# Optimization experiments

Measured on AMD Instinct MI355X. Metric: run time of the kernel, lower is better.

Reference implementation:

```python
import jax, jax.numpy as jnp
import numpy as np

N_PATCHES = 14
PS = 16            # patch size: 224 / 14
C, H_IMG, W_IMG = 3, 224, 224
HIDDEN = 768
HEADS = 12
DH = HIDDEN // HEADS
BLOCKS = 12
MLP = 4 * HIDDEN
OUT = 1000
SEQ = N_PATCHES ** 2 + 1  # 197
BATCH = 64


def get_positional_embeddings(seq_len, d):
    # sin(i/10000^(j/d)) for even j, cos(i/10000^((j-1)/d)) for odd j
    i = jnp.arange(seq_len, dtype=jnp.float32)[:, None]
    j = jnp.arange(d)[None, :]
    even = (j % 2 == 0)
    expo = jnp.where(even, j, j - 1).astype(jnp.float32) / d
    ang = i / (10000.0 ** expo)
    return jnp.where(even, jnp.sin(ang), jnp.cos(ang))


def layernorm(x, g, b, eps=1e-5):
    mu = x.mean(-1, keepdims=True)
    var = ((x - mu) ** 2).mean(-1, keepdims=True)
    return (x - mu) / jnp.sqrt(var + eps) * g + b


def mhsa(x, qw, qb, kw, kb, vw, vb):
    # x: [B,S,HIDDEN]; per-head linears qw/kw/vw: [H,DH,DH] (torch Linear weight layout)
    B, S, _ = x.shape
    xh = x.reshape(B, S, HEADS, DH)
    q = jnp.einsum('bshd,hed->bshe', xh, qw) + qb
    k = jnp.einsum('bshd,hed->bshe', xh, kw) + kb
    v = jnp.einsum('bshd,hed->bshe', xh, vw) + vb
    scores = jnp.einsum('bshe,bthe->bhst', q, k) / jnp.sqrt(jnp.float32(DH))
    attn = jax.nn.softmax(scores, axis=-1)
    out = jnp.einsum('bhst,bthe->bshe', attn, v)
    return out.reshape(B, S, HIDDEN)


def vit_block(x, p):
    ln1_g, ln1_b, qw, qb, kw, kb, vw, vb, ln2_g, ln2_b, w1, b1, w2, b2 = p
    x = x + mhsa(layernorm(x, ln1_g, ln1_b), qw, qb, kw, kb, vw, vb)
    h = layernorm(x, ln2_g, ln2_b)
    h = jax.nn.gelu(h @ w1.T + b1, approximate=False) @ w2.T + b2
    return x + h


def patchify(images):
    # [N,C,H,W] -> [N, n_patches^2, C*PS*PS], channel-major within each patch
    n = images.shape[0]
    x = images.reshape(n, C, N_PATCHES, PS, N_PATCHES, PS)
    x = x.transpose(0, 2, 4, 1, 3, 5)  # n, pi, pj, c, ps, ps
    return x.reshape(n, N_PATCHES * N_PATCHES, C * PS * PS)


def setup_inputs() -> dict:
    key = jax.random.key(0)
    ks = jax.random.split(key, 20)
    s = 0.02
    return {
        'images': jax.random.normal(ks[0], (BATCH, C, H_IMG, W_IMG), jnp.float32),
        'mapper_w': jax.random.normal(ks[1], (HIDDEN, C * PS * PS), jnp.float32) * s,
        'mapper_b': jnp.zeros((HIDDEN,), jnp.float32),
        'cls_token': jax.random.uniform(ks[2], (1, HIDDEN), jnp.float32),
        'ln1_g': jnp.ones((BLOCKS, HIDDEN), jnp.float32),
        'ln1_b': jnp.zeros((BLOCKS, HIDDEN), jnp.float32),
        'qw': jax.random.normal(ks[3], (BLOCKS, HEADS, DH, DH), jnp.float32) * s,
        'qb': jnp.zeros((BLOCKS, HEADS, DH), jnp.float32),
        'kw': jax.random.normal(ks[4], (BLOCKS, HEADS, DH, DH), jnp.float32) * s,
        'kb': jnp.zeros((BLOCKS, HEADS, DH), jnp.float32),
        'vw': jax.random.normal(ks[5], (BLOCKS, HEADS, DH, DH), jnp.float32) * s,
        'vb': jnp.zeros((BLOCKS, HEADS, DH), jnp.float32),
        'ln2_g': jnp.ones((BLOCKS, HIDDEN), jnp.float32),
        'ln2_b': jnp.zeros((BLOCKS, HIDDEN), jnp.float32),
        'w1': jax.random.normal(ks[6], (BLOCKS, MLP, HIDDEN), jnp.float32) * s,
        'b1': jnp.zeros((BLOCKS, MLP), jnp.float32),
        'w2': jax.random.normal(ks[7], (BLOCKS, HIDDEN, MLP), jnp.float32) * s,
        'b2': jnp.zeros((BLOCKS, HIDDEN), jnp.float32),
        'head_w': jax.random.normal(ks[8], (OUT, HIDDEN), jnp.float32) * s,
        'head_b': jnp.zeros((OUT,), jnp.float32),
    }


def reference(images, mapper_w, mapper_b, cls_token, ln1_g, ln1_b, qw, qb, kw, kb,
              vw, vb, ln2_g, ln2_b, w1, b1, w2, b2, head_w, head_b):
    n = images.shape[0]
    patches = patchify(images)
    tokens = patches @ mapper_w.T + mapper_b                      # [B, 196, HIDDEN]
    cls = jnp.broadcast_to(cls_token[None], (n, 1, HIDDEN))
    tokens = jnp.concatenate([cls, tokens], axis=1)               # [B, 197, HIDDEN]
    out = tokens + get_positional_embeddings(SEQ, HIDDEN)[None]

    stacked = (ln1_g, ln1_b, qw, qb, kw, kb, vw, vb, ln2_g, ln2_b, w1, b1, w2, b2)

    def step(x, p):
        return vit_block(x, p), None

    out, _ = jax.lax.scan(step, out, stacked)
    cls_out = out[:, 0]                                           # [B, HIDDEN]
    return jax.nn.softmax(cls_out @ head_w.T + head_b, axis=-1)
```

## Files before the change

kernel.cpp:

```cpp
#include <hip/hip_runtime.h>
#include <cstdint>
#include <cstddef>
#include <cstdio>

using u16 = unsigned short;
using u32 = unsigned int;

typedef __attribute__((ext_vector_type(8))) __bf16 bf16x8;
typedef __attribute__((ext_vector_type(4))) float f32x4;

struct alignas(16) U128 { u32 w[4]; };
struct alignas(16) F4   { float x[4]; };
struct alignas(8)  US4  { u16 h[4]; };

#define DEVFN static __device__ __forceinline__

DEVFN u16 f2bf(float x) {
  union { float f; u32 u; } v; v.f = x;
  u32 r = v.u + 0x7fffu + ((v.u >> 16) & 1u);
  return (u16)(r >> 16);
}

DEVFN bf16x8 ld16(const u16* p) { return __builtin_bit_cast(bf16x8, *(const U128*)p); }

DEVFN f32x4 mfma16(bf16x8 a, bf16x8 b, f32x4 c) {
  return __builtin_amdgcn_mfma_f32_16x16x32_bf16(a, b, c, 0, 0, 0);
}

DEVFN void gload_lds16(const u16* g, u16* l) {
  __builtin_amdgcn_global_load_lds(
      (const __attribute__((address_space(1))) void*)g,
      (__attribute__((address_space(3))) void*)l, 16, 0, 0);
}

DEVFN float gelu(float x) {
  float z = fabsf(x) * 0.70710678118f;
  float t = __builtin_amdgcn_rcpf(1.f + 0.3275911f * z);
  float p = t * (0.254829592f + t * (-0.284496736f + t * (1.421413741f +
            t * (-1.453152027f + t * 1.061405429f))));
  float e = __expf(-z * z);
  float erfz = 1.f - p * e;
  erfz = copysignf(erfz, x);
  return 0.5f * x * (1.f + erfz);
}

constexpr int SEQL   = 197;
constexpr int NB     = 64;
constexpr int NH     = 12;
constexpr int MROWS  = NB * SEQL;
constexpr int MPAD   = 12672;
constexpr int MPAD2  = 12800;
constexpr int MPATCH = NB * 196;
constexpr int SP     = 208;
constexpr int SP2    = 224;
constexpr int BHN    = NB * NH;

constexpr size_t OFF_X    = 0;
constexpr size_t OFF_ALN  = OFF_X    + (size_t)MPAD * 768 * 4;
constexpr size_t OFF_H    = OFF_ALN  + (size_t)MPAD2 * 768 * 2;
constexpr size_t OFF_WQKV = OFF_H    + (size_t)MPAD2 * 3072 * 2;
constexpr size_t OFF_W1   = OFF_WQKV + (size_t)2304 * 768 * 2;
constexpr size_t OFF_W2   = OFF_W1   + (size_t)3072 * 768 * 2;
constexpr size_t OFF_WMAP = OFF_W2   + (size_t)3072 * 768 * 2;
constexpr size_t OFF_Q    = OFF_WMAP + (size_t)768 * 768 * 2;
constexpr size_t OFF_K    = OFF_Q    + (size_t)BHN * SP * 64 * 2;
constexpr size_t OFF_VT   = OFF_K    + (size_t)BHN * SP * 64 * 2;
constexpr size_t OFF_PAT  = OFF_VT   + (size_t)BHN * 64 * SP2 * 2;
constexpr size_t OFF_POS  = OFF_PAT  + (size_t)MPATCH * 768 * 2;
constexpr size_t WS_NEED  = OFF_POS  + (size_t)SEQL * 768 * 4;

__global__ void zero_kernel(u32* __restrict__ p, long n) {
  long i = (long)blockIdx.x * 256 + threadIdx.x;
  long stride = (long)gridDim.x * 256;
  for (; i < n; i += stride) p[i] = 0u;
}

__global__ void cvt_kernel(const float* __restrict__ src, u16* __restrict__ dst, int n) {
  int i = blockIdx.x * 256 + threadIdx.x;
  if (i < n) dst[i] = f2bf(src[i]);
}

__global__ void pos_kernel(float* __restrict__ pos) {
  int i = blockIdx.x * 256 + threadIdx.x;
  if (i >= SEQL * 768) return;
  int s = i / 768, j = i - s * 768;
  float expo = (float)(j & ~1) * (1.0f / 768.0f);
  float ang  = (float)s * expf(-expo * logf(10000.0f));
  pos[i] = (j & 1) ? cosf(ang) : sinf(ang);
}

__global__ void cls_kernel(const float* __restrict__ cls, const float* __restrict__ pos,
                           float* __restrict__ X) {
  int b = blockIdx.x;
  for (int c = threadIdx.x; c < 768; c += 256)
    X[(size_t)b * SEQL * 768 + c] = cls[c] + pos[c];
}

__global__ void patchify_kernel(const float* __restrict__ img, u16* __restrict__ out) {
  int i = blockIdx.x * 256 + threadIdx.x;
  if (i >= MPATCH * 768) return;
  int m = i / 768, k = i - m * 768;
  int b = m / 196, p = m - b * 196;
  int py = p / 14, px = p - py * 14;
  int c = k >> 8, rem = k & 255, iy = rem >> 4, ix = rem & 15;
  float v = img[(((size_t)b * 3 + c) * 224 + py * 16 + iy) * 224 + px * 16 + ix];
  out[i] = f2bf(v);
}

__global__ void build_wqkv2(const float* __restrict__ qw, const float* __restrict__ kw,
                            const float* __restrict__ vw, u16* __restrict__ W, int blk) {
  int i = blockIdx.x * 256 + threadIdx.x;
  if (i >= 2304 * 128) return;
  int n = i >> 7, kk = i & 127;
  int p = n / 768, ef = n - p * 768;
  int h = ef >> 6, e = ef & 63;
  float v = 0.f;
  if ((kk >> 6) == (h & 1)) {
    int d = kk & 63;
    const float* w = (p == 0) ? qw : (p == 1) ? kw : vw;
    v = w[(((size_t)blk * NH + h) * 64 + e) * 64 + d];
  }
  W[i] = f2bf(v);
}

__global__ __launch_bounds__(256) void ln_kernel(const float* __restrict__ X,
    const float* __restrict__ g, const float* __restrict__ b, u16* __restrict__ out) {
  int row  = blockIdx.x * 4 + (threadIdx.x >> 6);
  int lane = threadIdx.x & 63;
  const float* x = X + (size_t)row * 768 + lane * 12;
  F4 a0 = *(const F4*)(x);
  F4 a1 = *(const F4*)(x + 4);
  F4 a2 = *(const F4*)(x + 8);
  float v[12];
  #pragma unroll
  for (int j = 0; j < 4; ++j) { v[j] = a0.x[j]; v[4 + j] = a1.x[j]; v[8 + j] = a2.x[j]; }
  float s = 0.f, q = 0.f;
  #pragma unroll
  for (int j = 0; j < 12; ++j) { s += v[j]; q += v[j] * v[j]; }
  #pragma unroll
  for (int d = 1; d < 64; d <<= 1) { s += __shfl_xor(s, d); q += __shfl_xor(q, d); }
  float mu  = s * (1.f / 768.f);
  float var = q * (1.f / 768.f) - mu * mu;
  float rs  = rsqrtf(var + 1e-5f);
  const float* gp = g + lane * 12;
  const float* bp = b + lane * 12;
  u16* op = out + (size_t)row * 768 + lane * 12;
  u16 o[12];
  #pragma unroll
  for (int j = 0; j < 12; ++j) o[j] = f2bf((v[j] - mu) * rs * gp[j] + bp[j]);
  #pragma unroll
  for (int c = 0; c < 3; ++c) {
    US4 w; w.h[0] = o[c*4]; w.h[1] = o[c*4+1]; w.h[2] = o[c*4+2]; w.h[3] = o[c*4+3];
    *(US4*)(op + c * 4) = w;
  }
}

enum { EPI_PATCH = 0, EPI_QKV = 1, EPI_GELU = 2, EPI_RESID = 3 };

template<int EPI>
__global__ __launch_bounds__(512, 2) void gemm256(
    const u16* __restrict__ A, const u16* __restrict__ B, int K, int Mb, int Nb,
    const float* __restrict__ e0, float* __restrict__ f0, u16* __restrict__ o0) {
  __shared__ u16 Ab[2][256 * 64];
  __shared__ u16 Bb[2][256 * 64];
  const int tid = threadIdx.x;
  const int wave = tid >> 6, lane = tid & 63;
  const int fr = lane & 15, fg = lane >> 4;
  const int nwg = Mb * Nb;
  {
    int q = nwg >> 3, r = nwg & 7;
    int xcd = (int)blockIdx.x & 7, pos = (int)blockIdx.x >> 3;
    int wg = (xcd < r ? xcd * (q + 1) : r * (q + 1) + (xcd - r) * q) + pos;
    __builtin_amdgcn_sched_barrier(0);
    ((int*)&Ab[0][0])[0] = 0;
    (void)wg;
    int bm_ = wg % Mb, bn_ = wg / Mb;
    #define BM_ bm_
    #define BN_ bn_
    const int srow = wave * 8 + (lane >> 3);
    const int gcol = ((lane & 7) ^ (lane >> 3)) * 8;
    const u16* gA = A + (size_t)(BM_ * 256 + srow) * K + gcol;
    const u16* gB = B + (size_t)(BN_ * 256 + srow) * K + gcol;
    u16* lA = &Ab[0][0] + wave * 512;
    u16* lB = &Bb[0][0] + wave * 512;
    const int nt = K >> 6;
    const int wm2 = wave >> 2, wn4 = wave & 3;
    const int sloA = (wm2 * 128 + fr) * 64;
    const int sloB = (wn4 * 64 + fr) * 64;
    const int sx = fr & 7;

    auto STAGE = [&](int b, int t) {
      const u16* a = gA + t * 64;
      const u16* bb = gB + t * 64;
      u16* la = lA + b * 0 + (size_t)0;
      (void)la;
      #pragma unroll
      for (int s = 0; s < 4; ++s) {
        gload_lds16(a + (size_t)s * 64 * K, &Ab[b][0] + wave * 512 + s * 4096);
        gload_lds16(bb + (size_t)s * 64 * K, &Bb[b][0] + wave * 512 + s * 4096);
      }
    };

    f32x4 acc[8][4] = {};
    STAGE(0, 0);
    for (int t = 0; t < nt; ++t) {
      if (t + 1 < nt) {
        STAGE((t + 1) & 1, t + 1);
        asm volatile("s_waitcnt vmcnt(8)" ::: "memory");
      } else {
        asm volatile("s_waitcnt vmcnt(0)" ::: "memory");
      }
      __builtin_amdgcn_s_barrier();
      const u16* ab = &Ab[t & 1][0];
      const u16* bbuf = &Bb[t & 1][0];
      #pragma unroll
      for (int ks = 0; ks < 2; ++ks) {
        const int sl = ((ks * 4 + fg) ^ sx) * 8;
        bf16x8 af[8], bfv[4];
        #pragma unroll
        for (int i = 0; i < 8; ++i) af[i] = ld16(ab + sloA + i * 16 * 64 + sl);
        #pragma unroll
        for (int j = 0; j < 4; ++j) bfv[j] = ld16(bbuf + sloB + j * 16 * 64 + sl);
        __builtin_amdgcn_s_setprio(1);
        #pragma unroll
        for (int i = 0; i < 8; ++i)
          #pragma unroll
          for (int j = 0; j < 4; ++j)
            acc[i][j] = mfma16(af[i], bfv[j], acc[i][j]);
        __builtin_amdgcn_s_setprio(0);
      }
      __builtin_amdgcn_s_barrier();
    }
    #pragma unroll
    for (int i = 0; i < 8; ++i) {
      #pragma unroll
      for (int r = 0; r < 4; ++r) {
        const int m = BM_ * 256 + wm2 * 128 + i * 16 + fg * 4 + r;
        if constexpr (EPI == EPI_GELU) {
          u16* hrow = o0 + (size_t)m * 3072;
          #pragma unroll
          for (int j = 0; j < 4; ++j) {
            const int n = BN_ * 256 + wn4 * 64 + j * 16 + fr;
            hrow[n] = f2bf(gelu(acc[i][j][r] + e0[n]));
          }
        } else {
          if (m < MROWS) {
            float* xrow = f0 + (size_t)m * 768;
            #pragma unroll
            for (int j = 0; j < 4; ++j) {
              const int n = BN_ * 256 + wn4 * 64 + j * 16 + fr;
              xrow[n] += acc[i][j][r] + e0[n];
            }
          }
        }
      }
    }
    #undef BM_
    #undef BN_
  }
}

template<int EPI>
__global__ __launch_bounds__(256) void gemm_bt(
    const u16* __restrict__ A, const u16* __restrict__ B, int K, int lda, int ldb,
    const float* __restrict__ e0, const float* __restrict__ e1, const float* __restrict__ e2,
    float* __restrict__ f0, const float* __restrict__ f1,
    u16* __restrict__ o0, u16* __restrict__ o1, u16* __restrict__ o2) {
  __shared__ u16 Ab[2][128 * 32];
  __shared__ u16 Bb[2][128 * 32];
  const int tid  = threadIdx.x;
  const int wave = tid >> 6, lane = tid & 63;
  const int bm = blockIdx.x, bn = blockIdx.y;
  const int fr = lane & 15, fg = lane >> 4;
  if constexpr (EPI == EPI_QKV) A += (bn % 6) * 128;
  const int srow = wave * 16 + (lane >> 2);
  const int gcol = ((lane & 3) ^ ((lane >> 3) & 3)) * 8;
  const u16* gA = A + (size_t)(bm * 128 + srow) * lda + gcol;
  const u16* gB = B + (size_t)(bn * 128 + srow) * ldb + gcol;
  const int wm = (wave >> 1) * 64, wn = (wave & 1) * 64;
  const int sx = (fr >> 1) & 3;
  const int nt = K >> 5;

  auto STAGE = [&](int b, int t) {
    #pragma unroll
    for (int s = 0; s < 2; ++s) {
      gload_lds16(gA + t * 32 + (size_t)s * 64 * lda, &Ab[b][0] + wave * 512 + s * 2048);
      gload_lds16(gB + t * 32 + (size_t)s * 64 * ldb, &Bb[b][0] + wave * 512 + s * 2048);
    }
  };

  f32x4 acc[4][4] = {};
  STAGE(0, 0);
  for (int t = 0; t < nt; ++t) {
    if (t + 1 < nt) {
      STAGE((t + 1) & 1, t + 1);
      asm volatile("s_waitcnt vmcnt(4)" ::: "memory");
    } else {
      asm volatile("s_waitcnt vmcnt(0)" ::: "memory");
    }
    __builtin_amdgcn_s_barrier();
    const u16* ab = &Ab[t & 1][0];
    const u16* bbuf = &Bb[t & 1][0];
    const int sl = (fg ^ sx) * 8;
    bf16x8 af[4], bfv[4];
    #pragma unroll
    for (int i = 0; i < 4; ++i) af[i]  = ld16(ab + (wm + i * 16 + fr) * 32 + sl);
    #pragma unroll
    for (int j = 0; j < 4; ++j) bfv[j] = ld16(bbuf + (wn + j * 16 + fr) * 32 + sl);
    __builtin_amdgcn_s_setprio(1);
    #pragma unroll
    for (int i = 0; i < 4; ++i)
      #pragma unroll
      for (int j = 0; j < 4; ++j)
        acc[i][j] = mfma16(af[i], bfv[j], acc[i][j]);
    __builtin_amdgcn_s_setprio(0);
    __builtin_amdgcn_s_barrier();
  }
  #pragma unroll
  for (int i = 0; i < 4; ++i) {
    #pragma unroll
    for (int r = 0; r < 4; ++r) {
      const int m = bm * 128 + wm + i * 16 + fg * 4 + r;
      if constexpr (EPI == EPI_PATCH) {
        const int bb = m / 196;
        const int s  = m - bb * 196 + 1;
        float* xrow = f0 + ((size_t)bb * SEQL + s) * 768;
        const float* prow = f1 + (size_t)s * 768;
        #pragma unroll
        for (int j = 0; j < 4; ++j) {
          const int n = bn * 128 + wn + j * 16 + fr;
          xrow[n] = acc[i][j][r] + e0[n] + prow[n];
        }
      } else if constexpr (EPI == EPI_QKV) {
        if (m < MROWS) {
          const int bb = m / 197;
          const int s  = m - bb * 197;
          #pragma unroll
          for (int j = 0; j < 4; ++j) {
            const int n = bn * 128 + wn + j * 16 + fr;
            const int p = n / 768;
            const int ef = n - p * 768;
            const int h = ef >> 6, e = ef & 63;
            const size_t bh = (size_t)bb * NH + h;
            if (p == 0)      o0[(bh * SP + s) * 64 + e] = f2bf((acc[i][j][r] + e0[ef]) * 0.125f);
            else if (p == 1) o1[(bh * SP + s) * 64 + e] = f2bf(acc[i][j][r] + e1[ef]);
            else             o2[(bh * 64 + e) * SP2 + s] = f2bf(acc[i][j][r] + e2[ef]);
          }
        }
      }
    }
  }
}

__global__ __launch_bounds__(256) void attn_kernel(const u16* __restrict__ Q,
    const u16* __restrict__ Km, const u16* __restrict__ Vt, float* __restrict__ X) {
  __shared__ u16  P[4][16 * SP2];
  __shared__ float sums[4][16];
  const int bh = blockIdx.x;
  const int b = bh / NH, h = bh - b * NH;
  const int wave = threadIdx.x >> 6, lane = threadIdx.x & 63;
  const int fr = lane & 15, fg = lane >> 4;
  const u16* Qb = Q  + (size_t)bh * SP * 64;
  const u16* Kb = Km + (size_t)bh * SP * 64;
  const u16* Vb = Vt + (size_t)bh * 64 * SP2;
  u16* Pl = &P[wave][0];
  for (int qt = wave; qt < 13; qt += 4) {
    const int s0 = qt * 16;
    bf16x8 qf0 = ld16(Qb + (size_t)(s0 + fr) * 64 + fg * 8);
    bf16x8 qf1 = ld16(Qb + (size_t)(s0 + fr) * 64 + 32 + fg * 8);
    f32x4 sc[13];
    #pragma unroll
    for (int tf = 0; tf < 13; ++tf) {
      f32x4 a = {0.f, 0.f, 0.f, 0.f};
      bf16x8 k0 = ld16(Kb + (size_t)(tf * 16 + fr) * 64 + fg * 8);
      bf16x8 k1 = ld16(Kb + (size_t)(tf * 16 + fr) * 64 + 32 + fg * 8);
      a = mfma16(qf0, k0, a);
      a = mfma16(qf1, k1, a);
      sc[tf] = a;
    }
    float mx[4] = {-3e38f, -3e38f, -3e38f, -3e38f};
    #pragma unroll
    for (int tf = 0; tf < 13; ++tf) {
      const bool ok = (tf * 16 + fr) < 197;
      #pragma unroll
      for (int r = 0; r < 4; ++r) {
        float v = ok ? sc[tf][r] : -3e38f;
        sc[tf][r] = v;
        mx[r] = fmaxf(mx[r], v);
      }
    }
    #pragma unroll
    for (int r = 0; r < 4; ++r)
      #pragma unroll
      for (int d = 1; d < 16; d <<= 1) mx[r] = fmaxf(mx[r], __shfl_xor(mx[r], d));
    float sm[4] = {0.f, 0.f, 0.f, 0.f};
    #pragma unroll
    for (int tf = 0; tf < 13; ++tf) {
      #pragma unroll
      for (int r = 0; r < 4; ++r) {
        float e = __expf(sc[tf][r] - mx[r]);
        sm[r] += e;
        Pl[(fg * 4 + r) * SP2 + tf * 16 + fr] = f2bf(e);
      }
    }
    #pragma unroll
    for (int r = 0; r < 4; ++r) {
      #pragma unroll
      for (int d = 1; d < 16; d <<= 1) sm[r] += __shfl_xor(sm[r], d);
      if (fr == 0) sums[wave][fg * 4 + r] = sm[r];
    }
    #pragma unroll
    for (int r = 0; r < 4; ++r) Pl[(fg * 4 + r) * SP2 + 208 + fr] = 0;
    f32x4 o[4] = {};
    #pragma unroll
    for (int ks = 0; ks < 7; ++ks) {
      bf16x8 pf = ld16(Pl + fr * SP2 + ks * 32 + fg * 8);
      #pragma unroll
      for (int ef = 0; ef < 4; ++ef) {
        bf16x8 vf = ld16(Vb + (size_t)(ef * 16 + fr) * SP2 + ks * 32 + fg * 8);
        o[ef] = mfma16(vf, pf, o[ef]);
      }
    }
    const float inv = 1.f / sums[wave][fr];
    const int s = s0 + fr;
    if (s < 197) {
      float* xp = X + ((size_t)b * SEQL + s) * 768 + h * 64;
      #pragma unroll
      for (int ef = 0; ef < 4; ++ef)
        #pragma unroll
        for (int r = 0; r < 4; ++r)
          xp[ef * 16 + fg * 4 + r] += o[ef][r] * inv;
    }
  }
}

__global__ __launch_bounds__(256) void head_kernel(const float* __restrict__ X,
    const float* __restrict__ hw, const float* __restrict__ hb, float* __restrict__ out) {
  __shared__ float xr[768];
  __shared__ float lg[1000];
  __shared__ float red[8];
  const int b = blockIdx.x, tid = threadIdx.x;
  for (int c = tid; c < 768; c += 256) xr[c] = X[(size_t)b * SEQL * 768 + c];
  __syncthreads();
  for (int n = tid; n < 1000; n += 256) {
    const F4* w4 = (const F4*)(hw + (size_t)n * 768);
    const F4* x4 = (const F4*)xr;
    float acc = hb[n];
    for (int k = 0; k < 192; ++k) {
      F4 w = w4[k]; F4 xv = x4[k];
      acc += w.x[0] * xv.x[0] + w.x[1] * xv.x[1] + w.x[2] * xv.x[2] + w.x[3] * xv.x[3];
    }
    lg[n] = acc;
  }
  __syncthreads();
  float m = -3e38f;
  for (int n = tid; n < 1000; n += 256) m = fmaxf(m, lg[n]);
  #pragma unroll
  for (int d = 1; d < 64; d <<= 1) m = fmaxf(m, __shfl_xor(m, d));
  if ((tid & 63) == 0) red[tid >> 6] = m;
  __syncthreads();
  m = fmaxf(fmaxf(red[0], red[1]), fmaxf(red[2], red[3]));
  float s = 0.f;
  for (int n = tid; n < 1000; n += 256) s += expf(lg[n] - m);
  #pragma unroll
  for (int d = 1; d < 64; d <<= 1) s += __shfl_xor(s, d);
  if ((tid & 63) == 0) red[4 + (tid >> 6)] = s;
  __syncthreads();
  s = red[4] + red[5] + red[6] + red[7];
  const float inv = 1.f / s;
  for (int n = tid; n < 1000; n += 256) out[(size_t)b * 1000 + n] = expf(lg[n] - m) * inv;
}

extern "C" void kernel_launch(void* const* d_in, const int* in_sizes, int n_in,
                              void* d_out, int out_size, void* d_ws, size_t ws_size,
                              hipStream_t stream) {
  (void)in_sizes; (void)n_in; (void)out_size;
  if (ws_size < WS_NEED) { printf("ws too small: %zu < %zu\n", ws_size, WS_NEED); return; }

  const float* images   = (const float*)d_in[0];
  const float* mapper_w = (const float*)d_in[1];
  const float* mapper_b = (const float*)d_in[2];
  const float* cls_tok  = (const float*)d_in[3];
  const float* ln1_g    = (const float*)d_in[4];
  const float* ln1_b    = (const float*)d_in[5];
  const float* qw       = (const float*)d_in[6];
  const float* qb       = (const float*)d_in[7];
  const float* kw       = (const float*)d_in[8];
  const float* kb       = (const float*)d_in[9];
  const float* vw       = (const float*)d_in[10];
  const float* vb       = (const float*)d_in[11];
  const float* ln2_g    = (const float*)d_in[12];
  const float* ln2_b    = (const float*)d_in[13];
  const float* w1       = (const float*)d_in[14];
  const float* b1       = (const float*)d_in[15];
  const float* w2       = (const float*)d_in[16];
  const float* b2       = (const float*)d_in[17];
  const float* head_w   = (const float*)d_in[18];
  const float* head_b   = (const float*)d_in[19];

  char* ws = (char*)d_ws;
  float* X    = (float*)(ws + OFF_X);
  u16*  Aln   = (u16*)(ws + OFF_ALN);
  u16*  Hb    = (u16*)(ws + OFF_H);
  u16*  Wqkv  = (u16*)(ws + OFF_WQKV);
  u16*  W1b   = (u16*)(ws + OFF_W1);
  u16*  W2b   = (u16*)(ws + OFF_W2);
  u16*  Wmap  = (u16*)(ws + OFF_WMAP);
  u16*  Qb    = (u16*)(ws + OFF_Q);
  u16*  Kb    = (u16*)(ws + OFF_K);
  u16*  Vtb   = (u16*)(ws + OFF_VT);
  u16*  Pat   = (u16*)(ws + OFF_PAT);
  float* Pos  = (float*)(ws + OFF_POS);

  zero_kernel<<<2048, 256, 0, stream>>>((u32*)Qb,  (long)(BHN * SP * 64 / 2));
  zero_kernel<<<2048, 256, 0, stream>>>((u32*)Kb,  (long)(BHN * SP * 64 / 2));
  zero_kernel<<<2048, 256, 0, stream>>>((u32*)Vtb, (long)(BHN * 64 * SP2 / 2));
  zero_kernel<<<64,   256, 0, stream>>>((u32*)(X + (size_t)MROWS * 768), (long)((MPAD - MROWS) * 768));
  zero_kernel<<<64,   256, 0, stream>>>((u32*)(Aln + (size_t)MPAD * 768), (long)((MPAD2 - MPAD) * 768 / 2));

  pos_kernel<<<(SEQL * 768 + 255) / 256, 256, 0, stream>>>(Pos);
  cvt_kernel<<<(768 * 768 + 255) / 256, 256, 0, stream>>>(mapper_w, Wmap, 768 * 768);
  patchify_kernel<<<(MPATCH * 768 + 255) / 256, 256, 0, stream>>>(images, Pat);
  cls_kernel<<<NB, 256, 0, stream>>>(cls_tok, Pos, X);

  gemm_bt<EPI_PATCH><<<dim3(MPATCH / 128, 768 / 128), 256, 0, stream>>>(
      Pat, Wmap, 768, 768, 768, mapper_b, nullptr, nullptr, X, Pos, nullptr, nullptr, nullptr);

  for (int blk = 0; blk < 12; ++blk) {
    ln_kernel<<<MPAD / 4, 256, 0, stream>>>(X, ln1_g + blk * 768, ln1_b + blk * 768, Aln);
    build_wqkv2<<<(2304 * 128 + 255) / 256, 256, 0, stream>>>(qw, kw, vw, Wqkv, blk);
    gemm_bt<EPI_QKV><<<dim3(MPAD / 128, 2304 / 128), 256, 0, stream>>>(
        Aln, Wqkv, 128, 768, 128, qb + blk * 768, kb + blk * 768, vb + blk * 768,
        nullptr, nullptr, Qb, Kb, Vtb);
    attn_kernel<<<BHN, 256, 0, stream>>>(Qb, Kb, Vtb, X);
    ln_kernel<<<MPAD / 4, 256, 0, stream>>>(X, ln2_g + blk * 768, ln2_b + blk * 768, Aln);
    cvt_kernel<<<(3072 * 768 + 255) / 256, 256, 0, stream>>>(w1 + (size_t)blk * 3072 * 768, W1b, 3072 * 768);
    gemm256<EPI_GELU><<<50 * 12, 512, 0, stream>>>(
        Aln, W1b, 768, 50, 12, b1 + blk * 3072, nullptr, Hb);
    cvt_kernel<<<(3072 * 768 + 255) / 256, 256, 0, stream>>>(w2 + (size_t)blk * 768 * 3072, W2b, 768 * 3072);
    gemm256<EPI_RESID><<<50 * 3, 512, 0, stream>>>(
        Hb, W2b, 3072, 50, 3, b2 + blk * 768, X, nullptr);
  }

  head_kernel<<<NB, 256, 0, stream>>>(X, head_w, head_b, (float*)d_out);
}
```

Before: 4.814 ms.

## Replace 256x256 MLP GEMM with 128x256 triple-buffered K=32 pipeline

Swaps the 512-thread 256x256-tile MLP GEMM for a 256-thread 128x256 tile kernel with three LDS stages, 32-wide K steps and two tiles in flight. The M padding drops from 12800 to 12672 rows, which removes the extra Aln zeroing and shrinks the workspace. The aim is to launch more workgroups (99x12 and 99x3 instead of 600 and 150) for better CU fill and latency hiding. In exchange each block does less reuse per tile and synchronises more often, with barriers every 32 K.

```diff
diff --git a/kernel.cpp b/kernel.cpp
--- a/kernel.cpp
+++ b/kernel.cpp
@@ -49,7 +49,6 @@
 constexpr int NH     = 12;
 constexpr int MROWS  = NB * SEQL;
 constexpr int MPAD   = 12672;
-constexpr int MPAD2  = 12800;
 constexpr int MPATCH = NB * 196;
 constexpr int SP     = 208;
 constexpr int SP2    = 224;
@@ -57,9 +56,9 @@
 
 constexpr size_t OFF_X    = 0;
 constexpr size_t OFF_ALN  = OFF_X    + (size_t)MPAD * 768 * 4;
-constexpr size_t OFF_H    = OFF_ALN  + (size_t)MPAD2 * 768 * 2;
-constexpr size_t OFF_WQKV = OFF_H    + (size_t)MPAD2 * 3072 * 2;
-constexpr size_t OFF_W1   = OFF_WQKV + (size_t)2304 * 768 * 2;
+constexpr size_t OFF_H    = OFF_ALN  + (size_t)MPAD * 768 * 2;
+constexpr size_t OFF_WQKV = OFF_H    + (size_t)MPAD * 3072 * 2;
+constexpr size_t OFF_W1   = OFF_WQKV + (size_t)2304 * 128 * 2;
 constexpr size_t OFF_W2   = OFF_W1   + (size_t)3072 * 768 * 2;
 constexpr size_t OFF_WMAP = OFF_W2   + (size_t)3072 * 768 * 2;
 constexpr size_t OFF_Q    = OFF_WMAP + (size_t)768 * 768 * 2;
@@ -158,105 +157,93 @@
 enum { EPI_PATCH = 0, EPI_QKV = 1, EPI_GELU = 2, EPI_RESID = 3 };
 
 template<int EPI>
-__global__ __launch_bounds__(512, 2) void gemm256(
-    const u16* __restrict__ A, const u16* __restrict__ B, int K, int Mb, int Nb,
+__global__ __launch_bounds__(256, 2) void gemm3s(
+    const u16* __restrict__ A, const u16* __restrict__ B, int K,
     const float* __restrict__ e0, float* __restrict__ f0, u16* __restrict__ o0) {
-  __shared__ u16 Ab[2][256 * 64];
-  __shared__ u16 Bb[2][256 * 64];
-  const int tid = threadIdx.x;
-  const int wave = tid >> 6, lane = tid & 63;
+  __shared__ u16 Ab[3][128 * 32];
+  __shared__ u16 Bb[3][256 * 32];
+  const int wave = threadIdx.x >> 6, lane = threadIdx.x & 63;
   const int fr = lane & 15, fg = lane >> 4;
-  const int nwg = Mb * Nb;
-  {
-    int q = nwg >> 3, r = nwg & 7;
-    int xcd = (int)blockIdx.x & 7, pos = (int)blockIdx.x >> 3;
-    int wg = (xcd < r ? xcd * (q + 1) : r * (q + 1) + (xcd - r) * q) + pos;
-    __builtin_amdgcn_sched_barrier(0);
-    ((int*)&Ab[0][0])[0] = 0;
-    (void)wg;
-    int bm_ = wg % Mb, bn_ = wg / Mb;
-    #define BM_ bm_
-    #define BN_ bn_
-    const int srow = wave * 8 + (lane >> 3);
-    const int gcol = ((lane & 7) ^ (lane >> 3)) * 8;
-    const u16* gA = A + (size_t)(BM_ * 256 + srow) * K + gcol;
-    const u16* gB = B + (size_t)(BN_ * 256 + srow) * K + gcol;
-    u16* lA = &Ab[0][0] + wave * 512;
-    u16* lB = &Bb[0][0] + wave * 512;
-    const int nt = K >> 6;
-    const int wm2 = wave >> 2, wn4 = wave & 3;
-    const int sloA = (wm2 * 128 + fr) * 64;
-    const int sloB = (wn4 * 64 + fr) * 64;
-    const int sx = fr & 7;
-
-    auto STAGE = [&](int b, int t) {
-      const u16* a = gA + t * 64;
-      const u16* bb = gB + t * 64;
-      u16* la = lA + b * 0 + (size_t)0;
-      (void)la;
-      #pragma unroll
-      for (int s = 0; s < 4; ++s) {
-        gload_lds16(a + (size_t)s * 64 * K, &Ab[b][0] + wave * 512 + s * 4096);
-        gload_lds16(bb + (size_t)s * 64 * K, &Bb[b][0] + wave * 512 + s * 4096);
-      }
-    };
-
-    f32x4 acc[8][4] = {};
-    STAGE(0, 0);
-    for (int t = 0; t < nt; ++t) {
-      if (t + 1 < nt) {
-        STAGE((t + 1) & 1, t + 1);
-        asm volatile("s_waitcnt vmcnt(8)" ::: "memory");
+  const int bm = blockIdx.x, bn = blockIdx.y;
+  const int srow = wave * 16 + (lane >> 2);
+  const int gcol = ((lane & 3) ^ ((lane >> 3) & 3)) * 8;
+  const u16* gA = A + (size_t)(bm * 128 + srow) * K + gcol;
+  const u16* gB = B + (size_t)(bn * 256 + srow) * K + gcol;
+  const int nt = K >> 5;
+  const int sl = (fg ^ ((fr >> 1) & 3)) * 8;
+
+  auto STAGE = [&](int c, int t) {
+    #pragma unroll
+    for (int s = 0; s < 2; ++s)
+      gload_lds16(gA + t * 32 + (size_t)(s * 64) * K, &Ab[c][0] + wave * 512 + s * 2048);
+    #pragma unroll
+    for (int s = 0; s < 4; ++s)
+      gload_lds16(gB + t * 32 + (size_t)(s * 64) * K, &Bb[c][0] + wave * 512 + s * 2048);
+  };
+
+  f32x4 acc[8][4] = {};
+
+  auto COMPUTE = [&](int c) {
+    const u16* ab = &Ab[c][0];
+    const u16* bb = &Bb[c][0];
+    bf16x8 af[8], bf[4];
+    #pragma unroll
+    for (int i = 0; i < 8; ++i) af[i] = ld16(ab + (i * 16 + fr) * 32 + sl);
+    #pragma unroll
+    for (int j = 0; j < 4; ++j) bf[j] = ld16(bb + (wave * 64 + j * 16 + fr) * 32 + sl);
+    __builtin_amdgcn_s_setprio(1);
+    #pragma unroll
+    for (int i = 0; i < 8; ++i)
+      #pragma unroll
+      for (int j = 0; j < 4; ++j)
+        acc[i][j] = mfma16(af[i], bf[j], acc[i][j]);
+    __builtin_amdgcn_s_setprio(0);
+  };
+
+  STAGE(0, 0);
+  STAGE(1, 1);
+  int cur = 0;
+  for (int t = 0; t + 2 < nt; ++t) {
+    int nxt = cur + 2; if (nxt >= 3) nxt -= 3;
+    STAGE(nxt, t + 2);
+    asm volatile("s_waitcnt vmcnt(12)" ::: "memory");
+    __builtin_amdgcn_s_barrier();
+    COMPUTE(cur);
+    __builtin_amdgcn_s_barrier();
+    cur = (cur + 1 == 3) ? 0 : cur + 1;
+  }
+  asm volatile("s_waitcnt vmcnt(6)" ::: "memory");
+  __builtin_amdgcn_s_barrier();
+  COMPUTE(cur);
+  __builtin_amdgcn_s_barrier();
+  cur = (cur + 1 == 3) ? 0 : cur + 1;
+  asm volatile("s_waitcnt vmcnt(0)" ::: "memory");
+  __builtin_amdgcn_s_barrier();
+  COMPUTE(cur);
+
+  #pragma unroll
+  for (int i = 0; i < 8; ++i) {
+    #pragma unroll
+    for (int r = 0; r < 4; ++r) {
+      const int m = bm * 128 + i * 16 + fg * 4 + r;
+      if constexpr (EPI == EPI_GELU) {
+        u16* hrow = o0 + (size_t)m * 3072;
+        #pragma unroll
+        for (int j = 0; j < 4; ++j) {
+          const int n = bn * 256 + wave * 64 + j * 16 + fr;
+          hrow[n] = f2bf(gelu(acc[i][j][r] + e0[n]));
+        }
       } else {
-        asm volatile("s_waitcnt vmcnt(0)" ::: "memory");
-      }
-      __builtin_amdgcn_s_barrier();
-      const u16* ab = &Ab[t & 1][0];
-      const u16* bbuf = &Bb[t & 1][0];
-      #pragma unroll
-      for (int ks = 0; ks < 2; ++ks) {
-        const int sl = ((ks * 4 + fg) ^ sx) * 8;
-        bf16x8 af[8], bfv[4];
-        #pragma unroll
-        for (int i = 0; i < 8; ++i) af[i] = ld16(ab + sloA + i * 16 * 64 + sl);
-        #pragma unroll
-        for (int j = 0; j < 4; ++j) bfv[j] = ld16(bbuf + sloB + j * 16 * 64 + sl);
-        __builtin_amdgcn_s_setprio(1);
-        #pragma unroll
-        for (int i = 0; i < 8; ++i)
-          #pragma unroll
-          for (int j = 0; j < 4; ++j)
-            acc[i][j] = mfma16(af[i], bfv[j], acc[i][j]);
-        __builtin_amdgcn_s_setprio(0);
-      }
-      __builtin_amdgcn_s_barrier();
-    }
-    #pragma unroll
-    for (int i = 0; i < 8; ++i) {
-      #pragma unroll
-      for (int r = 0; r < 4; ++r) {
-        const int m = BM_ * 256 + wm2 * 128 + i * 16 + fg * 4 + r;
-        if constexpr (EPI == EPI_GELU) {
-          u16* hrow = o0 + (size_t)m * 3072;
+        if (m < MROWS) {
+          float* xrow = f0 + (size_t)m * 768;
           #pragma unroll
           for (int j = 0; j < 4; ++j) {
-            const int n = BN_ * 256 + wn4 * 64 + j * 16 + fr;
-            hrow[n] = f2bf(gelu(acc[i][j][r] + e0[n]));
-          }
-        } else {
-          if (m < MROWS) {
-            float* xrow = f0 + (size_t)m * 768;
-            #pragma unroll
-            for (int j = 0; j < 4; ++j) {
-              const int n = BN_ * 256 + wn4 * 64 + j * 16 + fr;
-              xrow[n] += acc[i][j][r] + e0[n];
-            }
+            const int n = bn * 256 + wave * 64 + j * 16 + fr;
+            xrow[n] += acc[i][j][r] + e0[n];
           }
         }
       }
     }
-    #undef BM_
-    #undef BN_
   }
 }
 
@@ -516,7 +503,6 @@
   zero_kernel<<<2048, 256, 0, stream>>>((u32*)Kb,  (long)(BHN * SP * 64 / 2));
   zero_kernel<<<2048, 256, 0, stream>>>((u32*)Vtb, (long)(BHN * 64 * SP2 / 2));
   zero_kernel<<<64,   256, 0, stream>>>((u32*)(X + (size_t)MROWS * 768), (long)((MPAD - MROWS) * 768));
-  zero_kernel<<<64,   256, 0, stream>>>((u32*)(Aln + (size_t)MPAD * 768), (long)((MPAD2 - MPAD) * 768 / 2));
 
   pos_kernel<<<(SEQL * 768 + 255) / 256, 256, 0, stream>>>(Pos);
   cvt_kernel<<<(768 * 768 + 255) / 256, 256, 0, stream>>>(mapper_w, Wmap, 768 * 768);
@@ -535,11 +521,11 @@
     attn_kernel<<<BHN, 256, 0, stream>>>(Qb, Kb, Vtb, X);
     ln_kernel<<<MPAD / 4, 256, 0, stream>>>(X, ln2_g + blk * 768, ln2_b + blk * 768, Aln);
     cvt_kernel<<<(3072 * 768 + 255) / 256, 256, 0, stream>>>(w1 + (size_t)blk * 3072 * 768, W1b, 3072 * 768);
-    gemm256<EPI_GELU><<<50 * 12, 512, 0, stream>>>(
-        Aln, W1b, 768, 50, 12, b1 + blk * 3072, nullptr, Hb);
+    gemm3s<EPI_GELU><<<dim3(MPAD / 128, 3072 / 256), 256, 0, stream>>>(
+        Aln, W1b, 768, b1 + blk * 3072, nullptr, Hb);
     cvt_kernel<<<(3072 * 768 + 255) / 256, 256, 0, stream>>>(w2 + (size_t)blk * 768 * 3072, W2b, 768 * 3072);
-    gemm256<EPI_RESID><<<50 * 3, 512, 0, stream>>>(
-        Hb, W2b, 3072, 50, 3, b2 + blk * 768, X, nullptr);
+    gemm3s<EPI_RESID><<<dim3(MPAD / 128, 768 / 256), 256, 0, stream>>>(
+        Hb, W2b, 3072, b2 + blk * 768, X, nullptr);
   }
 
   head_kernel<<<NB, 256, 0, stream>>>(X, head_w, head_b, (float*)d_out);
```

After: 4.718 ms. 2.0% less time.
